# Kernel optimization log

Measured on AMD Instinct MI355X. Metric: run time of the kernel, lower is better.

Reference implementation:

```python
import jax, jax.numpy as jnp
import numpy as np

B, S, D, H = 1, 4096, 1024, 16
DH = D // H

def setup_inputs() -> dict:
    key = jax.random.key(0)
    ks = jax.random.split(key, 5)
    std = float(np.sqrt(2.0 / (D + D)))
    return {
        "x": jax.random.normal(ks[0], (B, S, D), dtype=jnp.float32),
        "Wq": jax.random.normal(ks[1], (D, D), dtype=jnp.float32) * std,
        "Wk": jax.random.normal(ks[2], (D, D), dtype=jnp.float32) * std,
        "Wv": jax.random.normal(ks[3], (D, D), dtype=jnp.float32) * std,
        "Wo": jax.random.normal(ks[4], (D, D), dtype=jnp.float32) * std,
    }

def reference(x, Wq, Wk, Wv, Wo):
    # projections: input @ W.T, then split heads: b s (h d) -> b h s d
    def split_heads(t):
        b, s, _ = t.shape
        return t.reshape(b, s, H, DH).transpose(0, 2, 1, 3)
    q = split_heads(x @ Wq.T)
    k = split_heads(x @ Wk.T)
    v = split_heads(x @ Wv.T)
    scale = 1.0 / jnp.sqrt(jnp.asarray(DH, dtype=x.dtype))
    scores = jnp.einsum("bhqd,bhkd->bhqk", q, k) * scale  # (b,h,s,s)
    # causal mask: allow k <= q
    causal = jnp.tril(jnp.ones((S, S), dtype=bool))
    scores = jnp.where(causal, scores, jnp.finfo(scores.dtype).min)
    attn = jax.nn.softmax(scores, axis=-1)
    out = jnp.einsum("bhqk,bhkd->bhqd", attn, v)  # (b,h,s,d)
    out = out.transpose(0, 2, 1, 3).reshape(B, S, D)  # b h s d -> b s (h d)
    return out @ Wo.T
```

## Files before the change

kernel.cpp:

```cpp
#include <hip/hip_runtime.h>
#include <math.h>

#define SEQ 4096
#define DM  1024
#define NH  16
#define DH  64
#define NS  4

typedef _Float16 h16;
typedef __attribute__((ext_vector_type(4))) _Float16 h16x4;
typedef __attribute__((ext_vector_type(8))) _Float16 h16x8;
typedef __attribute__((ext_vector_type(4))) float f32x4;

__device__ __forceinline__ void gload_lds16(const h16* g, h16* l) {
    __builtin_amdgcn_global_load_lds(
        (const __attribute__((address_space(1))) void*)g,
        (__attribute__((address_space(3))) void*)l, 16, 0, 0);
}

__global__ __launch_bounds__(256) void cvt_all(const float* __restrict__ x,
                                               const float* __restrict__ wq,
                                               const float* __restrict__ wk,
                                               const float* __restrict__ wv,
                                               const float* __restrict__ wo,
                                               h16* __restrict__ dst) {
    const size_t SD4 = (size_t)SEQ * DM / 4;
    const size_t DD4 = (size_t)DM * DM / 4;
    const size_t i = (size_t)blockIdx.x * 256 + threadIdx.x;
    const float* src;
    size_t off;
    if (i < SD4) { src = x; off = i; }
    else {
        const size_t j = i - SD4;
        const int wsel = (int)(j >> 18);
        off = j & (DD4 - 1);
        src = (wsel == 0) ? wq : (wsel == 1) ? wk : (wsel == 2) ? wv : wo;
    }
    const float4 v = ((const float4*)src)[off];
    h16x4 o = { (h16)v.x, (h16)v.y, (h16)v.z, (h16)v.w };
    ((h16x4*)dst)[i] = o;
}

#define GT 32

__global__ __launch_bounds__(256) void gemm_qkv(const h16* __restrict__ xh,
                                                const h16* __restrict__ Wq,
                                                const h16* __restrict__ Wk,
                                                const h16* __restrict__ Wv,
                                                h16* __restrict__ Qh,
                                                h16* __restrict__ Kh,
                                                h16* __restrict__ Vth,
                                                float scl) {
    __shared__ h16 As[2][128 * GT];
    __shared__ h16 Bs[2][128 * GT];

    const int z    = blockIdx.z;
    const h16* B   = (z == 0) ? Wq : (z == 1) ? Wk : Wv;
    const int t    = threadIdx.x;
    const int lane = t & 63;
    const int w    = t >> 6;
    const int wm   = (w >> 1) * 64;
    const int wn   = (w & 1) * 64;
    const int l15  = lane & 15;
    const int lq   = lane >> 4;
    const int lq8  = lq * 8;
    const int m0   = blockIdx.y * 128;
    const int n0   = blockIdx.x * 128;
    const int K = DM, M = SEQ, N = DM;

    const int srow = w * 16 + (lane >> 2);
    const int scol = (lane & 3) * 8;
    const h16* pa0 = xh + (size_t)(m0 + srow) * K + scol;
    const h16* pa1 = xh + (size_t)(m0 + 64 + srow) * K + scol;
    const h16* pb0 = B  + (size_t)(n0 + srow) * K + scol;
    const h16* pb1 = B  + (size_t)(n0 + 64 + srow) * K + scol;

    f32x4 acc[4][4] = {};

    for (int k0 = 0; k0 < K; k0 += 64) {
        __syncthreads();
        #pragma unroll
        for (int s = 0; s < 2; ++s) {
            const int ko = k0 + s * 32;
            gload_lds16(pa0 + ko, &As[s][w * 512]);
            gload_lds16(pa1 + ko, &As[s][2048 + w * 512]);
            gload_lds16(pb0 + ko, &Bs[s][w * 512]);
            gload_lds16(pb1 + ko, &Bs[s][2048 + w * 512]);
        }
        __syncthreads();

        #pragma unroll
        for (int s = 0; s < 2; ++s) {
            h16x8 af[4], bf[4];
            #pragma unroll
            for (int i = 0; i < 4; ++i)
                af[i] = *(const h16x8*)&As[s][(wm + i * 16 + l15) * GT + lq8];
            #pragma unroll
            for (int j = 0; j < 4; ++j)
                bf[j] = *(const h16x8*)&Bs[s][(wn + j * 16 + l15) * GT + lq8];
            #pragma unroll
            for (int i = 0; i < 4; ++i)
                #pragma unroll
                for (int j = 0; j < 4; ++j)
                    acc[i][j] = __builtin_amdgcn_mfma_f32_16x16x32_f16(af[i], bf[j], acc[i][j], 0, 0, 0);
        }
    }

    const int cr = wm + lq * 4;
    const int cc = wn + l15;
    if (z == 2) {
        #pragma unroll
        for (int i = 0; i < 4; ++i)
            #pragma unroll
            for (int j = 0; j < 4; ++j) {
                const int gm0 = m0 + cr + i * 16;
                const int gn  = n0 + cc + j * 16;
                h16x4 v = { (h16)acc[i][j][0], (h16)acc[i][j][1],
                            (h16)acc[i][j][2], (h16)acc[i][j][3] };
                *(h16x4*)(Vth + (size_t)gn * M + gm0) = v;
            }
    } else {
        h16* Og = (z == 0) ? Qh : Kh;
        const float e = (z == 0) ? scl : 1.0f;
        #pragma unroll
        for (int i = 0; i < 4; ++i)
            #pragma unroll
            for (int j = 0; j < 4; ++j)
                #pragma unroll
                for (int r = 0; r < 4; ++r) {
                    const int gm = m0 + cr + i * 16 + r;
                    const int gn = n0 + cc + j * 16;
                    Og[(size_t)gm * N + gn] = (h16)(acc[i][j][r] * e);
                }
    }
}

__global__ __launch_bounds__(256) void gemm_out(const h16* __restrict__ A,
                                                const h16* __restrict__ B,
                                                float* __restrict__ C) {
    __shared__ h16 As[2][64 * GT];
    __shared__ h16 Bs[2][128 * GT];

    const int t    = threadIdx.x;
    const int lane = t & 63;
    const int w    = t >> 6;
    const int wm   = (w >> 1) * 32;
    const int wn   = (w & 1) * 64;
    const int l15  = lane & 15;
    const int lq   = lane >> 4;
    const int lq8  = lq * 8;
    const int m0   = blockIdx.y * 64;
    const int n0   = blockIdx.x * 128;
    const int K = DM, N = DM;

    const int srow = w * 16 + (lane >> 2);
    const int scol = (lane & 3) * 8;
    const h16* pa0 = A + (size_t)(m0 + srow) * K + scol;
    const h16* pb0 = B + (size_t)(n0 + srow) * K + scol;
    const h16* pb1 = B + (size_t)(n0 + 64 + srow) * K + scol;

    f32x4 acc[2][4] = {};

    for (int k0 = 0; k0 < K; k0 += 64) {
        __syncthreads();
        #pragma unroll
        for (int s = 0; s < 2; ++s) {
            const int ko = k0 + s * 32;
            gload_lds16(pa0 + ko, &As[s][w * 512]);
            gload_lds16(pb0 + ko, &Bs[s][w * 512]);
            gload_lds16(pb1 + ko, &Bs[s][2048 + w * 512]);
        }
        __syncthreads();

        #pragma unroll
        for (int s = 0; s < 2; ++s) {
            h16x8 af[2], bf[4];
            #pragma unroll
            for (int i = 0; i < 2; ++i)
                af[i] = *(const h16x8*)&As[s][(wm + i * 16 + l15) * GT + lq8];
            #pragma unroll
            for (int j = 0; j < 4; ++j)
                bf[j] = *(const h16x8*)&Bs[s][(wn + j * 16 + l15) * GT + lq8];
            #pragma unroll
            for (int i = 0; i < 2; ++i)
                #pragma unroll
                for (int j = 0; j < 4; ++j)
                    acc[i][j] = __builtin_amdgcn_mfma_f32_16x16x32_f16(af[i], bf[j], acc[i][j], 0, 0, 0);
        }
    }

    const int cr = wm + lq * 4;
    const int cc = wn + l15;
    #pragma unroll
    for (int i = 0; i < 2; ++i)
        #pragma unroll
        for (int j = 0; j < 4; ++j)
            #pragma unroll
            for (int r = 0; r < 4; ++r)
                C[(size_t)(m0 + cr + i * 16 + r) * N + n0 + cc + j * 16] = acc[i][j][r];
}

#define AST 80
#define VST 72

__global__ __launch_bounds__(256, 6) void flash_attn_split(
        const h16* __restrict__ Qg, const h16* __restrict__ Kg,
        const h16* __restrict__ Vt, h16* __restrict__ OP,
        float* __restrict__ Mb, float* __restrict__ Lb) {
    __shared__ h16 Ks[64 * AST];
    __shared__ h16 Vs[64 * VST];

    const int qt   = 63 - (int)blockIdx.y;
    const int hh   = blockIdx.x;
    const int sp   = blockIdx.z;
    const int t    = threadIdx.x;
    const int lane = t & 63;
    const int w    = t >> 6;
    const int l15  = lane & 15;
    const int lq   = lane >> 4;
    const int lq8  = lq * 8;
    const int hc   = hh * DH;
    const int q0   = qt * 64;
    const int q_loc = w * 16 + l15;

    const int ntile = qt + 1;
    const int chunk = (ntile + NS - 1) / NS;
    const int kts   = sp * chunk;
    const int kte   = (kts + chunk < ntile) ? (kts + chunk) : ntile;

    const int r1 = t >> 3;
    const int r2 = r1 + 32;
    const int c1 = (t & 7) * 8;

    *(h16x8*)&Ks[r1 * AST + c1] = *(const h16x8*)(Qg + (size_t)(q0 + r1) * DM + hc + c1);
    *(h16x8*)&Ks[r2 * AST + c1] = *(const h16x8*)(Qg + (size_t)(q0 + r2) * DM + hc + c1);

    const int kb0 = kts * 64;
    h16x8 kv1 = *(const h16x8*)(Kg + (size_t)(kb0 + r1) * DM + hc + c1);
    h16x8 kv2 = *(const h16x8*)(Kg + (size_t)(kb0 + r2) * DM + hc + c1);
    h16x8 vv1 = *(const h16x8*)(Vt + (size_t)(hc + r1) * SEQ + kb0 + c1);
    h16x8 vv2 = *(const h16x8*)(Vt + (size_t)(hc + r2) * SEQ + kb0 + c1);

    __syncthreads();
    h16x8 qf[2];
    qf[0] = *(const h16x8*)&Ks[q_loc * AST + lq8];
    qf[1] = *(const h16x8*)&Ks[q_loc * AST + 32 + lq8];

    float m_st = -1e30f, l_st = 0.0f;
    f32x4 o[4] = {};

    for (int kt = kts; kt < kte; ++kt) {
        __syncthreads();
        *(h16x8*)&Ks[r1 * AST + c1] = kv1;
        *(h16x8*)&Ks[r2 * AST + c1] = kv2;
        *(h16x8*)&Vs[r1 * VST + c1] = vv1;
        *(h16x8*)&Vs[r2 * VST + c1] = vv2;
        __syncthreads();
        if (kt + 1 < kte) {
            const int k0n = (kt + 1) * 64;
            kv1 = *(const h16x8*)(Kg + (size_t)(k0n + r1) * DM + hc + c1);
            kv2 = *(const h16x8*)(Kg + (size_t)(k0n + r2) * DM + hc + c1);
            vv1 = *(const h16x8*)(Vt + (size_t)(hc + r1) * SEQ + k0n + c1);
            vv2 = *(const h16x8*)(Vt + (size_t)(hc + r2) * SEQ + k0n + c1);
        }

        f32x4 s[4] = {};
        #pragma unroll
        for (int kc = 0; kc < 2; ++kc)
            #pragma unroll
            for (int jj = 0; jj < 4; ++jj) {
                const h16x8 kf = *(const h16x8*)&Ks[(jj * 16 + l15) * AST + kc * 32 + lq8];
                s[jj] = __builtin_amdgcn_mfma_f32_16x16x32_f16(kf, qf[kc], s[jj], 0, 0, 0);
            }

        if (kt == qt) {
            #pragma unroll
            for (int jj = 0; jj < 4; ++jj)
                #pragma unroll
                for (int r = 0; r < 4; ++r)
                    if ((jj * 16 + lq * 4 + r) > q_loc) s[jj][r] = -1e30f;
        }
        float mx = -1e30f;
        #pragma unroll
        for (int jj = 0; jj < 4; ++jj)
            #pragma unroll
            for (int r = 0; r < 4; ++r)
                mx = fmaxf(mx, s[jj][r]);
        mx = fmaxf(mx, __shfl_xor(mx, 16, 64));
        mx = fmaxf(mx, __shfl_xor(mx, 32, 64));
        if (mx > m_st + 5.0f) {
            const float alpha = exp2f(m_st - mx);
            m_st = mx;
            l_st *= alpha;
            #pragma unroll
            for (int jj = 0; jj < 4; ++jj)
                #pragma unroll
                for (int r = 0; r < 4; ++r)
                    o[jj][r] *= alpha;
        }

        h16x4 pk[4];
        #pragma unroll
        for (int jj = 0; jj < 4; ++jj) {
            const float p0 = exp2f(s[jj][0] - m_st);
            const float p1 = exp2f(s[jj][1] - m_st);
            const float p2 = exp2f(s[jj][2] - m_st);
            const float p3 = exp2f(s[jj][3] - m_st);
            l_st += (p0 + p1) + (p2 + p3);
            pk[jj] = h16x4{ (h16)p0, (h16)p1, (h16)p2, (h16)p3 };
        }

        #pragma unroll
        for (int dd = 0; dd < 4; ++dd)
            #pragma unroll
            for (int jj = 0; jj < 4; ++jj) {
                const h16x4 vf = *(const h16x4*)&Vs[(dd * 16 + l15) * VST + jj * 16 + lq * 4];
                o[dd] = __builtin_amdgcn_mfma_f32_16x16x16f16(vf, pk[jj], o[dd], 0, 0, 0);
            }
    }

    l_st += __shfl_xor(l_st, 16, 64);
    l_st += __shfl_xor(l_st, 32, 64);

    h16* const op = OP + (size_t)sp * SEQ * DM;
    const size_t qg = (size_t)(q0 + q_loc) * DM + hc;
    #pragma unroll
    for (int jj = 0; jj < 4; ++jj) {
        h16x4 ov = { (h16)o[jj][0], (h16)o[jj][1],
                     (h16)o[jj][2], (h16)o[jj][3] };
        *(h16x4*)(op + qg + jj * 16 + lq * 4) = ov;
    }
    if (lq == 0) {
        const size_t mi = ((size_t)sp * NH + hh) * SEQ + q0 + q_loc;
        Mb[mi] = m_st;
        Lb[mi] = l_st;
    }
}

__global__ __launch_bounds__(256) void combine(const h16* __restrict__ OP,
                                               const float* __restrict__ Mb,
                                               const float* __restrict__ Lb,
                                               h16* __restrict__ AOh) {
    const int i  = blockIdx.x * 256 + threadIdx.x;
    const int q  = i >> 8;
    const int c4 = (i & 255) * 4;
    const int hh = c4 >> 6;

    float ms[NS], ls[NS];
    float mstar = -1e30f;
    #pragma unroll
    for (int s = 0; s < NS; ++s) {
        const size_t mi = ((size_t)s * NH + hh) * SEQ + q;
        ms[s] = Mb[mi];
        ls[s] = Lb[mi];
        mstar = fmaxf(mstar, ms[s]);
    }
    float L = 0.0f;
    float acc[4] = {};
    #pragma unroll
    for (int s = 0; s < NS; ++s) {
        const float ws = exp2f(ms[s] - mstar);
        L += ls[s] * ws;
        const h16x4 ov = *(const h16x4*)(OP + (size_t)s * SEQ * DM + (size_t)q * DM + c4);
        acc[0] += ws * (float)ov[0];
        acc[1] += ws * (float)ov[1];
        acc[2] += ws * (float)ov[2];
        acc[3] += ws * (float)ov[3];
    }
    const float inv = 1.0f / L;
    h16x4 r = { (h16)(acc[0] * inv), (h16)(acc[1] * inv),
                (h16)(acc[2] * inv), (h16)(acc[3] * inv) };
    *(h16x4*)(AOh + (size_t)q * DM + c4) = r;
}

extern "C" void kernel_launch(void* const* d_in, const int* in_sizes, int n_in,
                              void* d_out, int out_size, void* d_ws, size_t ws_size,
                              hipStream_t stream) {
    const float* x  = (const float*)d_in[0];
    const float* Wq = (const float*)d_in[1];
    const float* Wk = (const float*)d_in[2];
    const float* Wv = (const float*)d_in[3];
    const float* Wo = (const float*)d_in[4];
    float* out = (float*)d_out;

    const size_t SD = (size_t)SEQ * DM;
    const size_t DD = (size_t)DM * DM;

    h16* xh  = (h16*)d_ws;
    h16* wqh = xh + SD;
    h16* wkh = wqh + DD;
    h16* wvh = wkh + DD;
    h16* woh = wvh + DD;
    h16* Qh  = woh + DD;
    h16* Kh  = Qh + SD;
    h16* Vth = Kh + SD;
    h16* AOh = Vth + SD;
    h16* OP  = AOh + SD;
    float* Mb = (float*)(OP + (size_t)NS * SD);
    float* Lb = Mb + (size_t)NS * NH * SEQ;

    const dim3 blk(256);

    cvt_all<<<(int)((SD + 4 * DD) / 4 / 256), blk, 0, stream>>>(x, Wq, Wk, Wv, Wo, xh);

    const float SCL = 0.125f * 1.44269504088896340736f;

    gemm_qkv<<<dim3(DM / 128, SEQ / 128, 3), blk, 0, stream>>>(
        xh, wqh, wkh, wvh, Qh, Kh, Vth, SCL);

    flash_attn_split<<<dim3(NH, 64, NS), blk, 0, stream>>>(Qh, Kh, Vth, OP, Mb, Lb);

    combine<<<(int)(SD / 4 / 256), blk, 0, stream>>>(OP, Mb, Lb, AOh);

    gemm_out<<<dim3(DM / 128, SEQ / 64), blk, 0, stream>>>(AOh, woh, out);
}
```

Baseline: 230.1 us.

## Store Q/K/V head-blocked contiguous and XOR-swizzle K tile in LDS

The QKV projection epilogue now writes Q and K in a head-major [head][seq][64] layout and V^T in a [seq-tile][dim][64] tiled layout. Each attention tile load then reads contiguous 128-byte rows instead of strided rows across the full model dimension. The K/Q shared-memory tile also gets an XOR swizzle on its column offset to reduce LDS bank conflicts on the MFMA fragment reads. The new epilogue stores may be less coalesced, especially the scalar Q/K writes whose stride changes.

Measured after the change: 249.9 us. 1.09x slower.

```diff
diff --git a/kernel.cpp b/kernel.cpp
--- a/kernel.cpp
+++ b/kernel.cpp
@@ -66,7 +66,7 @@
     const int lq8  = lq * 8;
     const int m0   = blockIdx.y * 128;
     const int n0   = blockIdx.x * 128;
-    const int K = DM, M = SEQ, N = DM;
+    const int K = DM, M = SEQ;
 
     const int srow = w * 16 + (lane >> 2);
     const int scol = (lane & 3) * 8;
@@ -117,7 +117,7 @@
                 const int gn  = n0 + cc + j * 16;
                 h16x4 v = { (h16)acc[i][j][0], (h16)acc[i][j][1],
                             (h16)acc[i][j][2], (h16)acc[i][j][3] };
-                *(h16x4*)(Vth + (size_t)gn * M + gm0) = v;
+                *(h16x4*)(Vth + ((size_t)(gm0 >> 6) * DM + gn) * 64 + (gm0 & 63)) = v;
             }
     } else {
         h16* Og = (z == 0) ? Qh : Kh;
@@ -130,7 +130,7 @@
                 for (int r = 0; r < 4; ++r) {
                     const int gm = m0 + cr + i * 16 + r;
                     const int gn = n0 + cc + j * 16;
-                    Og[(size_t)gm * N + gn] = (h16)(acc[i][j][r] * e);
+                    Og[((size_t)(gn >> 6) * SEQ + gm) * 64 + (gn & 63)] = (h16)(acc[i][j][r] * e);
                 }
     }
 }
@@ -231,37 +231,43 @@
     const int r1 = t >> 3;
     const int r2 = r1 + 32;
     const int c1 = (t & 7) * 8;
-
-    *(h16x8*)&Ks[r1 * AST + c1] = *(const h16x8*)(Qg + (size_t)(q0 + r1) * DM + hc + c1);
-    *(h16x8*)&Ks[r2 * AST + c1] = *(const h16x8*)(Qg + (size_t)(q0 + r2) * DM + hc + c1);
+    const int sw  = ((r1 >> 2) & 3) << 3;
+    const int c1s = c1 ^ sw;
+    const int rsw = ((l15 >> 2) & 3) << 3;
+
+    const h16* Qb = Qg + (size_t)hh * SEQ * 64;
+    const h16* Kb = Kg + (size_t)hh * SEQ * 64;
+
+    *(h16x8*)&Ks[r1 * AST + c1s] = *(const h16x8*)(Qb + (size_t)(q0 + r1) * 64 + c1);
+    *(h16x8*)&Ks[r2 * AST + c1s] = *(const h16x8*)(Qb + (size_t)(q0 + r2) * 64 + c1);
 
     const int kb0 = kts * 64;
-    h16x8 kv1 = *(const h16x8*)(Kg + (size_t)(kb0 + r1) * DM + hc + c1);
-    h16x8 kv2 = *(const h16x8*)(Kg + (size_t)(kb0 + r2) * DM + hc + c1);
-    h16x8 vv1 = *(const h16x8*)(Vt + (size_t)(hc + r1) * SEQ + kb0 + c1);
-    h16x8 vv2 = *(const h16x8*)(Vt + (size_t)(hc + r2) * SEQ + kb0 + c1);
+    h16x8 kv1 = *(const h16x8*)(Kb + (size_t)(kb0 + r1) * 64 + c1);
+    h16x8 kv2 = *(const h16x8*)(Kb + (size_t)(kb0 + r2) * 64 + c1);
+    h16x8 vv1 = *(const h16x8*)(Vt + ((size_t)kts * DM + hc + r1) * 64 + c1);
+    h16x8 vv2 = *(const h16x8*)(Vt + ((size_t)kts * DM + hc + r2) * 64 + c1);
 
     __syncthreads();
     h16x8 qf[2];
-    qf[0] = *(const h16x8*)&Ks[q_loc * AST + lq8];
-    qf[1] = *(const h16x8*)&Ks[q_loc * AST + 32 + lq8];
+    qf[0] = *(const h16x8*)&Ks[q_loc * AST + (lq8 ^ rsw)];
+    qf[1] = *(const h16x8*)&Ks[q_loc * AST + ((32 + lq8) ^ rsw)];
 
     float m_st = -1e30f, l_st = 0.0f;
     f32x4 o[4] = {};
 
     for (int kt = kts; kt < kte; ++kt) {
         __syncthreads();
-        *(h16x8*)&Ks[r1 * AST + c1] = kv1;
-        *(h16x8*)&Ks[r2 * AST + c1] = kv2;
+        *(h16x8*)&Ks[r1 * AST + c1s] = kv1;
+        *(h16x8*)&Ks[r2 * AST + c1s] = kv2;
         *(h16x8*)&Vs[r1 * VST + c1] = vv1;
         *(h16x8*)&Vs[r2 * VST + c1] = vv2;
         __syncthreads();
         if (kt + 1 < kte) {
             const int k0n = (kt + 1) * 64;
-            kv1 = *(const h16x8*)(Kg + (size_t)(k0n + r1) * DM + hc + c1);
-            kv2 = *(const h16x8*)(Kg + (size_t)(k0n + r2) * DM + hc + c1);
-            vv1 = *(const h16x8*)(Vt + (size_t)(hc + r1) * SEQ + k0n + c1);
-            vv2 = *(const h16x8*)(Vt + (size_t)(hc + r2) * SEQ + k0n + c1);
+            kv1 = *(const h16x8*)(Kb + (size_t)(k0n + r1) * 64 + c1);
+            kv2 = *(const h16x8*)(Kb + (size_t)(k0n + r2) * 64 + c1);
+            vv1 = *(const h16x8*)(Vt + ((size_t)(kt + 1) * DM + hc + r1) * 64 + c1);
+            vv2 = *(const h16x8*)(Vt + ((size_t)(kt + 1) * DM + hc + r2) * 64 + c1);
         }
 
         f32x4 s[4] = {};
@@ -269,7 +275,7 @@
         for (int kc = 0; kc < 2; ++kc)
             #pragma unroll
             for (int jj = 0; jj < 4; ++jj) {
-                const h16x8 kf = *(const h16x8*)&Ks[(jj * 16 + l15) * AST + kc * 32 + lq8];
+                const h16x8 kf = *(const h16x8*)&Ks[(jj * 16 + l15) * AST + ((kc * 32 + lq8) ^ rsw)];
                 s[jj] = __builtin_amdgcn_mfma_f32_16x16x32_f16(kf, qf[kc], s[jj], 0, 0, 0);
             }
 
```
